# Kernel optimization log

Hardware: AMD Instinct MI355X
Metric: run time of the kernel (lower is better)

The kernel has to match this reference:

```python
import jax
import jax.numpy as jnp
import numpy as np
from jax import lax

B = 4096        # batch
DATA = 16       # data_dim (control channels)
HID = 64        # hidden_dim
VFW = 128       # vf_hidden_dim
LAB = 10        # label_dim
T = 201         # number of time points in ts (span [0,1])
DT0 = 0.01      # fixed step size -> 100 Heun steps over [0,1]
N_STEPS = 100


def _linear_init(key, out_f, in_f):
    kw, kb = jax.random.split(key)
    lim = 1.0 / np.sqrt(in_f)
    w = jax.random.uniform(kw, (out_f, in_f), minval=-lim, maxval=lim, dtype=jnp.float32)
    b = jax.random.uniform(kb, (out_f,), minval=-lim, maxval=lim, dtype=jnp.float32)
    return w, b


def setup_inputs() -> dict:
    key = jax.random.key(0)
    ks = jax.random.split(key, 8)
    ts = jnp.linspace(0.0, 1.0, T, dtype=jnp.float32)
    coeffs = jax.random.normal(ks[0], (T - 1, DATA, 4), dtype=jnp.float32) * 0.1
    x0 = jax.random.normal(ks[1], (B, DATA), dtype=jnp.float32)
    lin1_w, lin1_b = _linear_init(ks[2], HID, DATA)
    mlp_w0, mlp_b0 = _linear_init(ks[3], VFW, HID)
    mlp_w1, mlp_b1 = _linear_init(ks[4], VFW, VFW)
    mlp_w2, mlp_b2 = _linear_init(ks[5], HID * DATA, VFW)
    lin2_w, lin2_b = _linear_init(ks[6], LAB, HID)
    return dict(ts=ts, coeffs=coeffs, x0=x0,
                lin1_w=lin1_w, lin1_b=lin1_b,
                mlp_w0=mlp_w0, mlp_b0=mlp_b0,
                mlp_w1=mlp_w1, mlp_b1=mlp_b1,
                mlp_w2=mlp_w2, mlp_b2=mlp_b2,
                lin2_w=lin2_w, lin2_b=lin2_b)


def reference(ts, coeffs, x0, lin1_w, lin1_b, mlp_w0, mlp_b0, mlp_w1, mlp_b1,
              mlp_w2, mlp_b2, lin2_w, lin2_b):
    def control_deriv(t):
        # cubic spline segment lookup: coeffs[idx] is (DATA, 4)
        idx = jnp.clip(jnp.searchsorted(ts[1:], t), 0, T - 2)
        dt = t - ts[idx]
        c = coeffs[idx]
        return c[:, 0] + dt * (c[:, 1] + dt * (c[:, 2] + dt * c[:, 3]))  # (DATA,)

    def vector_field(t, y):
        # MLP: HID -> VFW -> VFW -> HID*DATA (relu, relu, tanh)
        h = jax.nn.relu(y @ mlp_w0.T + mlp_b0)
        h = jax.nn.relu(h @ mlp_w1.T + mlp_b1)
        h = jnp.tanh(h @ mlp_w2.T + mlp_b2)
        vf = h.reshape(-1, HID, DATA)            # (B, HID, DATA)
        cd = control_deriv(t)                    # (DATA,)
        return jnp.einsum('bhd,d->bh', vf, cd)   # dy/dt, (B, HID)

    y0 = x0 @ lin1_w.T + lin1_b                  # (B, HID)
    t0 = ts[0]
    t1 = ts[-1]
    dt = (t1 - t0) / N_STEPS                     # == DT0 for [0,1] span

    def step(carry, _):
        y, t = carry
        k1 = vector_field(t, y)
        k2 = vector_field(t + dt, y + dt * k1)
        y_next = y + 0.5 * dt * (k1 + k2)        # Heun (explicit trapezoidal)
        return (y_next, t + dt), None

    (y_final, _), _ = lax.scan(step, (y0, t0), None, length=N_STEPS)
    logits = y_final @ lin2_w.T + lin2_b
    return jax.nn.softmax(logits, axis=-1)       # (B, LAB)
```

## Files before the change

kernel.cpp:

```cpp
#include <hip/hip_runtime.h>

#define BTOT   4096
#define DATA   16
#define HID    64
#define VFW    128
#define LAB    10
#define TPTS   201
#define NSEG   200
#define NSTEPS 100
#define MT     16
#define NBLK   (BTOT / MT)
#define YS     68

typedef __attribute__((ext_vector_type(8))) short short8;
typedef __attribute__((ext_vector_type(4))) float f32x4;
typedef __attribute__((ext_vector_type(2))) unsigned uint2v;

#define LOG2E  1.4426950408889634f
#define K2L    (2.0f * LOG2E)

__device__ __forceinline__ short f2bf(float f) {
    unsigned u = __builtin_bit_cast(unsigned, f);
    u = (u + 0x7FFFu + ((u >> 16) & 1u)) >> 16;
    return (short)u;
}

__device__ __forceinline__ unsigned cvt_pk_bf16(float lo, float hi) {
    unsigned r;
    asm("v_cvt_pk_bf16_f32 %0, %1, %2" : "=v"(r) : "v"(lo), "v"(hi));
    return r;
}

__device__ __forceinline__ float exp2_raw(float x) {
#if __has_builtin(__builtin_amdgcn_exp2f)
    return __builtin_amdgcn_exp2f(x);
#else
    return exp2f(x);
#endif
}

__global__ void pack_w(const float* __restrict__ W, short* __restrict__ outp,
                       int N, int K) {
    int tid = blockIdx.x * blockDim.x + threadIdx.x;
    int KS = K >> 5;
    int total = (N >> 4) * KS * 64;
    if (tid >= total) return;
    int ln = tid & 63;
    int fs = tid >> 6;
    int ks = fs % KS;
    int nt = fs / KS;
    int n  = nt * 16 + (ln & 15);
    int k0 = ks * 32 + (ln >> 4) * 8;
    const float* src = W + n * K + k0;
    short8 v;
#pragma unroll
    for (int j = 0; j < 8; ++j) v[j] = f2bf(src[j]);
    *(((short8*)outp) + tid) = v;
}

__global__ __launch_bounds__(1024, 4) void cde_main(
    const float* __restrict__ ts_g,  const float* __restrict__ coeffs,
    const float* __restrict__ x0,    const float* __restrict__ lin1_w,
    const float* __restrict__ lin1_b,
    const float* __restrict__ b0g,   const float* __restrict__ b1g,
    const float* __restrict__ b2g,   const float* __restrict__ l2w,
    const float* __restrict__ l2b,
    const short8* __restrict__ w0p,  const short8* __restrict__ w1p,
    const short8* __restrict__ w2p,  float* __restrict__ out)
{
    __shared__ float ts_sh[TPTS];
    __shared__ float ttab[NSTEPS + 1];
    __shared__ float cdtab[(NSTEPS + 1) * DATA];
    __shared__ float cdqtab[(NSTEPS + 1) * 4];
    __shared__ float y32[MT * YS];
    __shared__ __align__(16) short ybf[MT * 72];
    __shared__ __align__(16) short h1bf[MT * 136];
    __shared__ __align__(16) short h2bf[MT * 136];
    __shared__ float b2s[HID * DATA];
    __shared__ __align__(16) short w0f[1024 * 8];
    __shared__ __align__(16) short w1f[2048 * 8];
    __shared__ float lgts[MT * 12];

    const int tid  = threadIdx.x;
    const int lane = tid & 63;
    const int wave = tid >> 6;
    const int lm   = lane & 15;
    const int lg   = lane >> 4;
    const int row0 = blockIdx.x * MT;

    for (int i = tid; i < TPTS; i += 1024) ts_sh[i] = ts_g[i];
    __syncthreads();

    const float dtv = (ts_sh[TPTS - 1] - ts_sh[0]) / 100.0f;
    const float half_dt = 0.5f * dtv;

    if (tid == 0) {
        float tv = ts_sh[0];
        ttab[0] = tv;
        for (int s = 0; s < NSTEPS; ++s) { tv = tv + dtv; ttab[s + 1] = tv; }
    }
    for (int i = tid; i < HID * DATA; i += 1024) b2s[i] = b2g[i];
    for (int i = tid; i < 1024; i += 1024) ((short8*)w0f)[i] = w0p[i];
    for (int i = tid; i < 2048; i += 1024) ((short8*)w1f)[i] = w1p[i];

    const int ycol = wave * 4 + lg;
    float yreg;
    {
        float s = lin1_b[ycol];
        const float* xr = x0 + (row0 + lm) * DATA;
        const float* wr = lin1_w + ycol * DATA;
#pragma unroll
        for (int k = 0; k < DATA; ++k) s += xr[k] * wr[k];
        yreg = s;
        ybf[lm * 72 + ycol] = f2bf(s);
    }
    __syncthreads();

    for (int idx = tid; idx < (NSTEPS + 1) * DATA; idx += 1024) {
        float tv = ttab[idx >> 4];
        int d = idx & 15;
        int g  = (int)(tv * 200.0f);
        int i0 = g - 2; i0 = i0 < 0 ? 0 : (i0 > 196 ? 196 : i0);
        float v0 = ts_sh[i0 + 1], v1 = ts_sh[i0 + 2], v2 = ts_sh[i0 + 3], v3 = ts_sh[i0 + 4];
        int aidx = i0 + (v0 < tv) + (v1 < tv) + (v2 < tv) + (v3 < tv);
        aidx = aidx > (NSEG - 1) ? (NSEG - 1) : aidx;
        float dtl = tv - ts_sh[aidx];
        const f32x4 cc = *(const f32x4*)(coeffs + (aidx * DATA + d) * 4);
        cdtab[idx] = cc[0] + dtl * (cc[1] + dtl * (cc[2] + dtl * cc[3]));
    }
    __syncthreads();
    for (int idx = tid; idx < (NSTEPS + 1) * 4; idx += 1024) {
        const f32x4 c = *(const f32x4*)&cdtab[idx * 4];
        cdqtab[idx] = (c[0] + c[1]) + (c[2] + c[3]);
    }

    short8 w2r[4][4];
#pragma unroll
    for (int i = 0; i < 4; ++i)
#pragma unroll
        for (int ks = 0; ks < 4; ++ks)
            w2r[i][ks] = w2p[((wave * 4 + i) * 4 + ks) * 64 + lane];
    const f32x4 bias4 = (wave < 8)
        ? *(const f32x4*)&b0g[wave * 16 + 4 * lg]
        : *(const f32x4*)&b1g[(wave - 8) * 16 + 4 * lg];
    __syncthreads();

    auto evalVF = [&](int tidx) -> float {
        if (wave < 8) {
            short8 yb0 = *(const short8*)&ybf[lm * 72 + 0  + lg * 8];
            short8 yb1 = *(const short8*)&ybf[lm * 72 + 32 + lg * 8];
            short8 ws0 = ((const short8*)w0f)[(wave * 2 + 0) * 64 + lane];
            short8 ws1 = ((const short8*)w0f)[(wave * 2 + 1) * 64 + lane];
            f32x4 a = bias4;
            f32x4 b = {0.f, 0.f, 0.f, 0.f};
            a = __builtin_amdgcn_mfma_f32_16x16x32_bf16(ws0, yb0, a, 0, 0, 0);
            b = __builtin_amdgcn_mfma_f32_16x16x32_bf16(ws1, yb1, b, 0, 0, 0);
            f32x4 acc1 = a + b;
            unsigned lo = cvt_pk_bf16(fmaxf(acc1[0], 0.f), fmaxf(acc1[1], 0.f));
            unsigned hi = cvt_pk_bf16(fmaxf(acc1[2], 0.f), fmaxf(acc1[3], 0.f));
            uint2v st; st[0] = lo; st[1] = hi;
            *(uint2v*)&h1bf[lm * 136 + wave * 16 + 4 * lg] = st;
        }
        __syncthreads();
        const f32x4 cdr = *(const f32x4*)&cdtab[tidx * DATA + 4 * lg];
        const float sumcd = cdqtab[tidx * 4 + lg];
        if (wave >= 8) {
            const int nt = wave - 8;
            f32x4 a = bias4;
            f32x4 b = {0.f, 0.f, 0.f, 0.f};
#pragma unroll
            for (int ks = 0; ks < 2; ++ks) {
                short8 h0 = *(const short8*)&h1bf[lm * 136 + (2 * ks) * 32 + lg * 8];
                short8 h1 = *(const short8*)&h1bf[lm * 136 + (2 * ks + 1) * 32 + lg * 8];
                short8 ws0 = ((const short8*)w1f)[(nt * 4 + 2 * ks) * 64 + lane];
                short8 ws1 = ((const short8*)w1f)[(nt * 4 + 2 * ks + 1) * 64 + lane];
                a = __builtin_amdgcn_mfma_f32_16x16x32_bf16(ws0, h0, a, 0, 0, 0);
                b = __builtin_amdgcn_mfma_f32_16x16x32_bf16(ws1, h1, b, 0, 0, 0);
            }
            f32x4 acc2 = a + b;
            unsigned lo = cvt_pk_bf16(fmaxf(acc2[0], 0.f), fmaxf(acc2[1], 0.f));
            unsigned hi = cvt_pk_bf16(fmaxf(acc2[2], 0.f), fmaxf(acc2[3], 0.f));
            uint2v st; st[0] = lo; st[1] = hi;
            *(uint2v*)&h2bf[lm * 136 + nt * 16 + 4 * lg] = st;
        }
        __syncthreads();
        short8 hb[4];
#pragma unroll
        for (int ks = 0; ks < 4; ++ks)
            hb[ks] = *(const short8*)&h2bf[lm * 136 + ks * 32 + lg * 8];
        float p0, p1, p2, p3;
#pragma unroll
        for (int i = 0; i < 4; ++i) {
            int nb = (wave * 4 + i) * 16 + 4 * lg;
            f32x4 acc = *(const f32x4*)&b2s[nb];
#pragma unroll
            for (int ks = 0; ks < 4; ++ks)
                acc = __builtin_amdgcn_mfma_f32_16x16x32_bf16(w2r[i][ks], hb[ks], acc, 0, 0, 0);
            float csum = 0.f;
#pragma unroll
            for (int r = 0; r < 4; ++r) {
                float e  = exp2_raw(acc[r] * K2L);
                float rc = __builtin_amdgcn_rcpf(e + 1.0f);
                csum = __builtin_fmaf(cdr[r], rc, csum);
            }
            float sv = __builtin_fmaf(csum, -2.0f, sumcd);
            if (i == 0) p0 = sv; else if (i == 1) p1 = sv;
            else if (i == 2) p2 = sv; else p3 = sv;
        }
        bool g1 = (lg & 1) != 0;
        float a4 = (lg & 2) ? p2 : p0;
        float b4 = (lg & 2) ? p3 : p1;
        float c4 = (lg & 2) ? p0 : p2;
        float d4 = (lg & 2) ? p1 : p3;
        float pg  = g1 ? b4 : a4;
        float pg1 = g1 ? a4 : b4;
        float pg2 = g1 ? d4 : c4;
        float pg3 = g1 ? c4 : d4;
        float s1  = pg  + __shfl_xor(pg1, 16);
        float s1b = pg2 + __shfl_xor(pg3, 16);
        return s1 + __shfl_xor(s1b, 32);
    };

    const int yboff = lm * 72 + ycol;
    for (int s = 0; s < NSTEPS; ++s) {
        float K1 = evalVF(s);
        ybf[yboff] = f2bf(__builtin_fmaf(dtv, K1, yreg));
        yreg = __builtin_fmaf(half_dt, K1, yreg);
        __syncthreads();
        float K2 = evalVF(s + 1);
        yreg = __builtin_fmaf(half_dt, K2, yreg);
        ybf[yboff] = f2bf(yreg);
        __syncthreads();
    }

    y32[lm * YS + ycol] = yreg;
    __syncthreads();
    if (tid < MT * LAB) {
        int m = tid / LAB, j = tid % LAB;
        float s = l2b[j];
        const float* wr = l2w + j * HID;
#pragma unroll
        for (int h = 0; h < HID; ++h) s += y32[m * YS + h] * wr[h];
        lgts[m * 12 + j] = s;
    }
    __syncthreads();
    if (tid < MT) {
        int m = tid;
        float mx = lgts[m * 12];
#pragma unroll
        for (int j = 1; j < LAB; ++j) mx = fmaxf(mx, lgts[m * 12 + j]);
        float e[LAB]; float sum = 0.f;
#pragma unroll
        for (int j = 0; j < LAB; ++j) { e[j] = __expf(lgts[m * 12 + j] - mx); sum += e[j]; }
#pragma unroll
        for (int j = 0; j < LAB; ++j) out[(row0 + m) * LAB + j] = e[j] / sum;
    }
}

extern "C" void kernel_launch(void* const* d_in, const int* in_sizes, int n_in,
                              void* d_out, int out_size, void* d_ws, size_t ws_size,
                              hipStream_t stream) {
    (void)in_sizes; (void)n_in; (void)out_size; (void)ws_size;
    const float* ts     = (const float*)d_in[0];
    const float* coeffs = (const float*)d_in[1];
    const float* x0     = (const float*)d_in[2];
    const float* lin1_w = (const float*)d_in[3];
    const float* lin1_b = (const float*)d_in[4];
    const float* w0     = (const float*)d_in[5];
    const float* b0     = (const float*)d_in[6];
    const float* w1     = (const float*)d_in[7];
    const float* b1     = (const float*)d_in[8];
    const float* w2     = (const float*)d_in[9];
    const float* b2     = (const float*)d_in[10];
    const float* l2w    = (const float*)d_in[11];
    const float* l2b    = (const float*)d_in[12];

    short* w0pack = (short*)d_ws;
    short* w1pack = (short*)((char*)d_ws + 16384);
    short* w2pack = (short*)((char*)d_ws + 49152);

    pack_w<<<dim3(4),  256, 0, stream>>>(w0, w0pack, 128, 64);
    pack_w<<<dim3(8),  256, 0, stream>>>(w1, w1pack, 128, 128);
    pack_w<<<dim3(64), 256, 0, stream>>>(w2, w2pack, 1024, 128);
    cde_main<<<dim3(NBLK), 1024, 0, stream>>>(ts, coeffs, x0, lin1_w, lin1_b,
        b0, b1, b2, l2w, l2b,
        (const short8*)w0pack, (const short8*)w1pack, (const short8*)w2pack,
        (float*)d_out);
}
```

Measured before the change: 393.2 us.

## Swizzle LDS activation layout, fold tanh scale into W2, use hardware bf16 convert

Applies an XOR swizzle to the LDS row layout of the hidden and y activation buffers so the MFMA operand reads and the scattered stores spread across banks. It also folds the 2*log2(e) tanh scale into the packed W2 weights and the b2 bias, which removes a multiply per element in the inner loop. The layer-1 MFMA now chains into one accumulator instead of two, and the y writeback uses the hardware v_cvt_pk_bf16 instruction instead of software rounding. Scaling W2 before the bf16 conversion changes the rounding slightly.

After: 399.3 us. No clear change (+1.5%).

```diff
diff --git a/kernel.cpp b/kernel.cpp
--- a/kernel.cpp
+++ b/kernel.cpp
@@ -39,8 +39,15 @@
 #endif
 }
 
+__device__ __forceinline__ int hidx(int row, int kb, int off) {
+    return row * 136 + ((kb ^ (row & 3)) << 5) + off;
+}
+__device__ __forceinline__ int yidx(int row, int kb, int off) {
+    return row * 72 + ((kb ^ (row & 1)) << 5) + off;
+}
+
 __global__ void pack_w(const float* __restrict__ W, short* __restrict__ outp,
-                       int N, int K) {
+                       int N, int K, float scale) {
     int tid = blockIdx.x * blockDim.x + threadIdx.x;
     int KS = K >> 5;
     int total = (N >> 4) * KS * 64;
@@ -54,7 +61,7 @@
     const float* src = W + n * K + k0;
     short8 v;
 #pragma unroll
-    for (int j = 0; j < 8; ++j) v[j] = f2bf(src[j]);
+    for (int j = 0; j < 8; ++j) v[j] = f2bf(scale * src[j]);
     *(((short8*)outp) + tid) = v;
 }
 
@@ -99,7 +106,7 @@
         ttab[0] = tv;
         for (int s = 0; s < NSTEPS; ++s) { tv = tv + dtv; ttab[s + 1] = tv; }
     }
-    for (int i = tid; i < HID * DATA; i += 1024) b2s[i] = b2g[i];
+    for (int i = tid; i < HID * DATA; i += 1024) b2s[i] = K2L * b2g[i];
     for (int i = tid; i < 1024; i += 1024) ((short8*)w0f)[i] = w0p[i];
     for (int i = tid; i < 2048; i += 1024) ((short8*)w1f)[i] = w1p[i];
 
@@ -112,7 +119,7 @@
 #pragma unroll
         for (int k = 0; k < DATA; ++k) s += xr[k] * wr[k];
         yreg = s;
-        ybf[lm * 72 + ycol] = f2bf(s);
+        ybf[yidx(lm, ycol >> 5, ycol & 31)] = f2bf(s);
     }
     __syncthreads();
 
@@ -147,19 +154,18 @@
 
     auto evalVF = [&](int tidx) -> float {
         if (wave < 8) {
-            short8 yb0 = *(const short8*)&ybf[lm * 72 + 0  + lg * 8];
-            short8 yb1 = *(const short8*)&ybf[lm * 72 + 32 + lg * 8];
+            short8 yb0 = *(const short8*)&ybf[yidx(lm, 0, lg * 8)];
+            short8 yb1 = *(const short8*)&ybf[yidx(lm, 1, lg * 8)];
             short8 ws0 = ((const short8*)w0f)[(wave * 2 + 0) * 64 + lane];
             short8 ws1 = ((const short8*)w0f)[(wave * 2 + 1) * 64 + lane];
-            f32x4 a = bias4;
-            f32x4 b = {0.f, 0.f, 0.f, 0.f};
-            a = __builtin_amdgcn_mfma_f32_16x16x32_bf16(ws0, yb0, a, 0, 0, 0);
-            b = __builtin_amdgcn_mfma_f32_16x16x32_bf16(ws1, yb1, b, 0, 0, 0);
-            f32x4 acc1 = a + b;
+            f32x4 acc1 = bias4;
+            acc1 = __builtin_amdgcn_mfma_f32_16x16x32_bf16(ws0, yb0, acc1, 0, 0, 0);
+            acc1 = __builtin_amdgcn_mfma_f32_16x16x32_bf16(ws1, yb1, acc1, 0, 0, 0);
+            int col = wave * 16 + 4 * lg;
             unsigned lo = cvt_pk_bf16(fmaxf(acc1[0], 0.f), fmaxf(acc1[1], 0.f));
             unsigned hi = cvt_pk_bf16(fmaxf(acc1[2], 0.f), fmaxf(acc1[3], 0.f));
             uint2v st; st[0] = lo; st[1] = hi;
-            *(uint2v*)&h1bf[lm * 136 + wave * 16 + 4 * lg] = st;
+            *(uint2v*)&h1bf[hidx(lm, col >> 5, col & 31)] = st;
         }
         __syncthreads();
         const f32x4 cdr = *(const f32x4*)&cdtab[tidx * DATA + 4 * lg];
@@ -170,24 +176,25 @@
             f32x4 b = {0.f, 0.f, 0.f, 0.f};
 #pragma unroll
             for (int ks = 0; ks < 2; ++ks) {
-                short8 h0 = *(const short8*)&h1bf[lm * 136 + (2 * ks) * 32 + lg * 8];
-                short8 h1 = *(const short8*)&h1bf[lm * 136 + (2 * ks + 1) * 32 + lg * 8];
+                short8 h0 = *(const short8*)&h1bf[hidx(lm, 2 * ks + 0, lg * 8)];
+                short8 h1 = *(const short8*)&h1bf[hidx(lm, 2 * ks + 1, lg * 8)];
                 short8 ws0 = ((const short8*)w1f)[(nt * 4 + 2 * ks) * 64 + lane];
                 short8 ws1 = ((const short8*)w1f)[(nt * 4 + 2 * ks + 1) * 64 + lane];
                 a = __builtin_amdgcn_mfma_f32_16x16x32_bf16(ws0, h0, a, 0, 0, 0);
                 b = __builtin_amdgcn_mfma_f32_16x16x32_bf16(ws1, h1, b, 0, 0, 0);
             }
             f32x4 acc2 = a + b;
+            int col = nt * 16 + 4 * lg;
             unsigned lo = cvt_pk_bf16(fmaxf(acc2[0], 0.f), fmaxf(acc2[1], 0.f));
             unsigned hi = cvt_pk_bf16(fmaxf(acc2[2], 0.f), fmaxf(acc2[3], 0.f));
             uint2v st; st[0] = lo; st[1] = hi;
-            *(uint2v*)&h2bf[lm * 136 + nt * 16 + 4 * lg] = st;
+            *(uint2v*)&h2bf[hidx(lm, col >> 5, col & 31)] = st;
         }
         __syncthreads();
         short8 hb[4];
 #pragma unroll
         for (int ks = 0; ks < 4; ++ks)
-            hb[ks] = *(const short8*)&h2bf[lm * 136 + ks * 32 + lg * 8];
+            hb[ks] = *(const short8*)&h2bf[hidx(lm, ks, lg * 8)];
         float p0, p1, p2, p3;
 #pragma unroll
         for (int i = 0; i < 4; ++i) {
@@ -199,7 +206,7 @@
             float csum = 0.f;
 #pragma unroll
             for (int r = 0; r < 4; ++r) {
-                float e  = exp2_raw(acc[r] * K2L);
+                float e  = exp2_raw(acc[r]);
                 float rc = __builtin_amdgcn_rcpf(e + 1.0f);
                 csum = __builtin_fmaf(cdr[r], rc, csum);
             }
@@ -221,15 +228,15 @@
         return s1 + __shfl_xor(s1b, 32);
     };
 
-    const int yboff = lm * 72 + ycol;
+    const int yboff = yidx(lm, ycol >> 5, ycol & 31);
     for (int s = 0; s < NSTEPS; ++s) {
         float K1 = evalVF(s);
-        ybf[yboff] = f2bf(__builtin_fmaf(dtv, K1, yreg));
+        ybf[yboff] = (short)cvt_pk_bf16(__builtin_fmaf(dtv, K1, yreg), 0.f);
         yreg = __builtin_fmaf(half_dt, K1, yreg);
         __syncthreads();
         float K2 = evalVF(s + 1);
         yreg = __builtin_fmaf(half_dt, K2, yreg);
-        ybf[yboff] = f2bf(yreg);
+        ybf[yboff] = (short)cvt_pk_bf16(yreg, 0.f);
         __syncthreads();
     }
 
@@ -279,9 +286,9 @@
     short* w1pack = (short*)((char*)d_ws + 16384);
     short* w2pack = (short*)((char*)d_ws + 49152);
 
-    pack_w<<<dim3(4),  256, 0, stream>>>(w0, w0pack, 128, 64);
-    pack_w<<<dim3(8),  256, 0, stream>>>(w1, w1pack, 128, 128);
-    pack_w<<<dim3(64), 256, 0, stream>>>(w2, w2pack, 1024, 128);
+    pack_w<<<dim3(4),  256, 0, stream>>>(w0, w0pack, 128, 64,  1.0f);
+    pack_w<<<dim3(8),  256, 0, stream>>>(w1, w1pack, 128, 128, 1.0f);
+    pack_w<<<dim3(64), 256, 0, stream>>>(w2, w2pack, 1024, 128, K2L);
     cde_main<<<dim3(NBLK), 1024, 0, stream>>>(ts, coeffs, x0, lin1_w, lin1_b,
         b0, b1, b2, l2w, l2b,
         (const short8*)w0pack, (const short8*)w1pack, (const short8*)w2pack,
```
